# Optimization experiments

Measured on AMD Instinct MI355X. Metric: run time of the kernel, lower is better.

Reference implementation:

```python
import jax, jax.numpy as jnp
import numpy as np

N_NODES = 50000
N_EDGES = 400000
DIMS = 32
HEADS = 6
FEAT = DIMS * HEADS  # 192
NEG_SLOPE = 0.2  # PyG GATv2Conv default


def glorot(key, shape):
    fan_in, fan_out = shape[0], shape[1]
    lim = jnp.sqrt(6.0 / (fan_in + fan_out))
    return jax.random.uniform(key, shape, jnp.float32, -lim, lim)


def setup_inputs() -> dict:
    key = jax.random.key(0)
    ks = jax.random.split(key, 10)
    x = jax.random.normal(ks[0], (N_NODES, FEAT), jnp.float32)
    edge_index = jax.random.randint(ks[1], (2, N_EDGES), 0, N_NODES, jnp.int32)
    edge_weights = jax.random.uniform(ks[2], (N_EDGES, 1), jnp.float32)
    W_l = glorot(ks[3], (FEAT, FEAT))   # lin_l: in -> heads*out
    b_l = jnp.zeros((FEAT,), jnp.float32)
    W_r = glorot(ks[4], (FEAT, FEAT))   # lin_r (share_weights=False)
    b_r = jnp.zeros((FEAT,), jnp.float32)
    W_edge = glorot(ks[5], (1, FEAT))   # lin_edge: edge_dim=1 -> heads*out, no bias
    att = glorot(ks[6], (HEADS, DIMS))  # attention vector per head
    bias = jnp.zeros((FEAT,), jnp.float32)
    return {"x": x, "edge_index": edge_index, "edge_weights": edge_weights,
            "W_l": W_l, "b_l": b_l, "W_r": W_r, "b_r": b_r,
            "W_edge": W_edge, "att": att, "bias": bias}


def gatv2_res(x, edge_index, edge_weights, W_l, b_l, W_r, b_r, W_edge, att, bias):
    N = x.shape[0]
    H, C = att.shape
    src0, dst0 = edge_index[0], edge_index[1]

    # add_self_loops with fill_value='mean': self-loop attr = mean of edge_attr over incoming edges
    cnt = jax.ops.segment_sum(jnp.ones((edge_weights.shape[0],), x.dtype), dst0, num_segments=N)
    loop_attr = jax.ops.segment_sum(edge_weights, dst0, num_segments=N) / jnp.maximum(cnt, 1.0)[:, None]
    loops = jnp.arange(N, dtype=src0.dtype)
    src = jnp.concatenate([src0, loops])
    dst = jnp.concatenate([dst0, loops])
    e_attr = jnp.concatenate([edge_weights, loop_attr], axis=0)  # [E+N, 1]

    x_l = (x @ W_l + b_l).reshape(N, H, C)  # source transform
    x_r = (x @ W_r + b_r).reshape(N, H, C)  # target transform
    e_emb = (e_attr @ W_edge).reshape(-1, H, C)

    # per-edge GATv2 score
    m = jax.nn.leaky_relu(x_l[src] + x_r[dst] + e_emb, NEG_SLOPE)  # [E+N, H, C]
    alpha = jnp.einsum('ehc,hc->eh', m, att)  # [E+N, H]

    # segment softmax over edges incident to each target node (self-loops guarantee coverage)
    amax = jax.lax.stop_gradient(jax.ops.segment_max(alpha, dst, num_segments=N))
    ex = jnp.exp(alpha - amax[dst])
    denom = jax.ops.segment_sum(ex, dst, num_segments=N)
    a = ex / denom[dst]  # [E+N, H]

    out = jax.ops.segment_sum(x_l[src] * a[..., None], dst, num_segments=N)  # [N, H, C]
    out = out.reshape(N, H * C) + bias

    # ResLayer: residual + ReLU (dropout = identity in eval mode)
    return jax.nn.relu(x + out)


def reference(x, edge_index, edge_weights, W_l, b_l, W_r, b_r, W_edge, att, bias):
    return gatv2_res(x, edge_index, edge_weights, W_l, b_l, W_r, b_r, W_edge, att, bias)
```

## Files before the change

kernel.cpp:

```cpp
#include <hip/hip_runtime.h>
#include <hip/hip_bf16.h>
#include <math.h>

#define N_NODES 50000
#define N_EDGES 400000
#define HEADS 6
#define DIMS 32
#define FEAT 192
#define NEG_SLOPE 0.2f

typedef __attribute__((ext_vector_type(8))) short short8;
typedef __attribute__((ext_vector_type(4))) float f32x4;

__device__ __forceinline__ unsigned short f2bu(float f) {
    __hip_bfloat16 h = __float2bfloat16(f);
    unsigned short u; __builtin_memcpy(&u, &h, 2); return u;
}
__device__ __forceinline__ float bu2f(unsigned short u) {
    return __uint_as_float(((unsigned)u) << 16);
}

#define XL_OFF    0
#define XR_OFF    19200000
#define WT_OFF    38400000
#define BLR_OFF   38547456
#define PAIR_OFF  38548992
#define DEG_OFF   41748992
#define SCAN_OFF  42148992
#define BSUM_OFF  42348992
#define BOFF_OFF  42350016
#define NB_SCAN ((N_NODES + 255) / 256)

__global__ __launch_bounds__(256) void k_count(const int* __restrict__ ei,
                                               int* __restrict__ deg,
                                               const float* __restrict__ Wl,
                                               const float* __restrict__ Wr,
                                               const float* __restrict__ bl,
                                               const float* __restrict__ br,
                                               short* __restrict__ Wt,
                                               float* __restrict__ blr) {
    int e = blockIdx.x * blockDim.x + threadIdx.x;
    if (e < N_EDGES) atomicAdd(&deg[ei[N_EDGES + e]], 1);
    if (e < 384 * FEAT) {
        int n = e / FEAT, k = e - n * FEAT;
        float v = (n < FEAT) ? Wl[k * FEAT + n] : Wr[k * FEAT + (n - FEAT)];
        Wt[n * FEAT + k] = (short)f2bu(v);
    }
    if (e < 384) blr[e] = (e < FEAT) ? bl[e] : br[e - FEAT];
}

__global__ __launch_bounds__(256) void k_scan1(const int* __restrict__ deg,
                                               int* __restrict__ scan,
                                               int* __restrict__ bsums) {
    int t = threadIdx.x;
    int i = blockIdx.x * 256 + t;
    int v = (i < N_NODES) ? deg[i] : 0;
    __shared__ int s[256];
    s[t] = v; __syncthreads();
    for (int off = 1; off < 256; off <<= 1) {
        int u = (t >= off) ? s[t - off] : 0;
        __syncthreads();
        s[t] += u;
        __syncthreads();
    }
    if (i < N_NODES) scan[i] = s[t];
    if (t == 255) bsums[blockIdx.x] = s[255];
}

__global__ __launch_bounds__(256) void k_scan2(int* __restrict__ bsums,
                                               int* __restrict__ boffs) {
    int t = threadIdx.x;
    int v = (t < NB_SCAN) ? bsums[t] : 0;
    __shared__ int s[256];
    s[t] = v; __syncthreads();
    for (int off = 1; off < 256; off <<= 1) {
        int u = (t >= off) ? s[t - off] : 0;
        __syncthreads();
        s[t] += u;
        __syncthreads();
    }
    boffs[t] = s[t] - v;
}

#define SCAT_BLOCKS ((N_EDGES + 383) / 384)
#define GEMM_BLOCKS (N_NODES / 16)
#define OSTRIDE 392
#define ASTRIDE 200
__global__ __launch_bounds__(384) void k_scatgemm(const int* __restrict__ ei,
                                                  const float* __restrict__ ew,
                                                  const int* __restrict__ scan,
                                                  const int* __restrict__ boffs,
                                                  int* __restrict__ deg,
                                                  int2* __restrict__ pair,
                                                  const float* __restrict__ x,
                                                  const short* __restrict__ Wt,
                                                  const float* __restrict__ blr,
                                                  unsigned short* __restrict__ xl,
                                                  unsigned short* __restrict__ xr) {
    __shared__ unsigned short sOut[16 * OSTRIDE];
    __shared__ unsigned short sA[16 * ASTRIDE];
    if (blockIdx.x < SCAT_BLOCKS) {
        int e = blockIdx.x * 384 + threadIdx.x;
        if (e < N_EDGES) {
            int d = ei[N_EDGES + e];
            int inclEnd = boffs[d >> 8] + scan[d];
            int old = atomicSub(&deg[d], 1);
            int2 p; p.x = ei[e]; p.y = __float_as_int(ew[e]);
            pair[inclEnd - old] = p;
        }
        return;
    }
    size_t row0 = (size_t)(blockIdx.x - SCAT_BLOCKS) * 16;

    {
        int q = threadIdx.x;
        int row = q / 24, k0 = (q - row * 24) * 8;
        const float* ap = x + (row0 + row) * FEAT + k0;
        float4 v0 = *(const float4*)ap;
        float4 v1 = *(const float4*)(ap + 4);
        unsigned short tmp[8];
        tmp[0] = f2bu(v0.x); tmp[1] = f2bu(v0.y); tmp[2] = f2bu(v0.z); tmp[3] = f2bu(v0.w);
        tmp[4] = f2bu(v1.x); tmp[5] = f2bu(v1.y); tmp[6] = f2bu(v1.z); tmp[7] = f2bu(v1.w);
        int kw = (k0 >> 1) ^ ((row & 7) << 2);
        *(uint4*)&sA[row * ASTRIDE + kw * 2] = *(const uint4*)tmp;
    }
    __syncthreads();

    int wv   = threadIdx.x >> 6;
    int lane = threadIdx.x & 63;
    int m    = lane & 15;
    int kg   = lane >> 4;
    int ncol0 = wv * 64;

    f32x4 acc0 = {0.f,0.f,0.f,0.f}, acc1 = acc0, acc2 = acc0, acc3 = acc0;

#pragma unroll
    for (int ks = 0; ks < 6; ks++) {
        int kb = ks * 32 + kg * 8;
        int kw = (kb >> 1) ^ ((m & 7) << 2);
        short8 af = *(const short8*)&sA[m * ASTRIDE + kw * 2];
        const short* wp = Wt + (size_t)(ncol0 + m) * FEAT + kb;
        short8 b0 = *(const short8*)(wp);
        short8 b1 = *(const short8*)(wp + 16 * FEAT);
        short8 b2 = *(const short8*)(wp + 32 * FEAT);
        short8 b3 = *(const short8*)(wp + 48 * FEAT);
        acc0 = __builtin_amdgcn_mfma_f32_16x16x32_bf16(af, b0, acc0, 0, 0, 0);
        acc1 = __builtin_amdgcn_mfma_f32_16x16x32_bf16(af, b1, acc1, 0, 0, 0);
        acc2 = __builtin_amdgcn_mfma_f32_16x16x32_bf16(af, b2, acc2, 0, 0, 0);
        acc3 = __builtin_amdgcn_mfma_f32_16x16x32_bf16(af, b3, acc3, 0, 0, 0);
    }

    f32x4 accs[4] = {acc0, acc1, acc2, acc3};
#pragma unroll
    for (int t4 = 0; t4 < 4; t4++) {
        int cc = ncol0 + t4 * 16 + m;
        float bv = blr[cc];
#pragma unroll
        for (int r = 0; r < 4; r++) {
            sOut[(kg * 4 + r) * OSTRIDE + cc] = f2bu(accs[t4][r] + bv);
        }
    }
    __syncthreads();
    for (int q = threadIdx.x; q < 768; q += 384) {
        int row = q / 48, p = q - row * 48;
        uint4 v = *(const uint4*)&sOut[row * OSTRIDE + p * 8];
        if (p < 24) *(uint4*)(xl + (row0 + row) * FEAT + p * 8) = v;
        else        *(uint4*)(xr + (row0 + row) * FEAT + (p - 24) * 8) = v;
    }
}

#define NPB 8
#define CEDGE 32
#define RS 100
#define APAD 36
__global__ __launch_bounds__(192) void k_node(const float* __restrict__ x,
                                              const float* __restrict__ bias,
                                              const float* __restrict__ att,
                                              const float* __restrict__ We,
                                              const int* __restrict__ scan,
                                              const int* __restrict__ boffs,
                                              const int2* __restrict__ pair,
                                              const unsigned short* __restrict__ xl,
                                              const unsigned short* __restrict__ xr,
                                              float* __restrict__ out) {
    __shared__ __align__(16) unsigned int sXL[CEDGE * RS];
    __shared__ __align__(16) unsigned int sXR[NPB * RS];
    __shared__ float sEx[CEDGE * HEADS];
    __shared__ float sExS[NPB * HEADS];
    __shared__ int   sSrc[2][CEDGE];
    __shared__ float sW[2][CEDGE];
    __shared__ int   sDst[2][CEDGE];
    __shared__ int   sStart[NPB + 1];
    __shared__ __align__(16) float sAttP[HEADS * APAD];
    __shared__ __align__(16) float sWeP[HEADS * APAD];
    __shared__ float sDen[NPB * HEADS];
    __shared__ float sWsm[NPB];

    int t = threadIdx.x;
    int h = t >> 5;
    int n0 = blockIdx.x * NPB;

    int gbase = boffs[n0 >> 8] + ((n0 & 255) ? scan[n0 - 1] : 0);
    int n8 = n0 + NPB;
    int gend = (n8 >= N_NODES) ? N_EDGES
             : (boffs[n8 >> 8] + ((n8 & 255) ? scan[n8 - 1] : 0));
    int etot = gend - gbase;
    int c0 = min(etot, CEDGE);

    if (t < c0) { int2 p = pair[gbase + t]; sSrc[0][t] = p.x; sW[0][t] = __int_as_float(p.y); }

    for (int q = t; q < HEADS * APAD; q += 192) {
        int hh = q / APAD, c = q - hh * APAD;
        if (c < 32) { sAttP[q] = att[hh * 32 + c]; sWeP[q] = We[hh * 32 + c]; }
    }
    if (t <= NPB) {
        int n = n0 + t;
        int st;
        if (n >= N_NODES) st = N_EDGES;
        else {
            int b = n >> 8;
            st = boffs[b] + ((n & 255) ? scan[n - 1] : 0);
        }
        sStart[t] = st;
    }
    if (t < NPB) {
        int n = n0 + t;
        int a = boffs[n >> 8] + ((n & 255) ? scan[n - 1] : 0);
        int n1 = n + 1;
        int b = (n1 >= N_NODES) ? N_EDGES
              : (boffs[n1 >> 8] + ((n1 & 255) ? scan[n1 - 1] : 0));
        int lo = a - gbase; if (lo < 0) lo = 0;
        int hi = b - gbase; if (hi > c0) hi = c0;
        for (int q = lo; q < hi; q++) sDst[0][q] = t;
    }
    {
        int nn = t / 24, p = t - nn * 24;
        *(uint4*)&sXR[nn * RS + p * 4] = ((const uint4*)(xr + (size_t)(n0 + nn) * FEAT))[p];
    }
    __syncthreads();

    float acc[NPB];
#pragma unroll
    for (int nn = 0; nn < NPB; nn++) acc[nn] = 0.f;
    float redR = 0.f;
    int nnD = t / HEADS, hhD = t - nnD * HEADS;

    int nch = (etot + CEDGE - 1) / CEDGE;
    for (int ci = 0; ci < nch; ci++) {
        int i0 = ci * CEDGE;
        int c  = min(etot - i0, CEDGE);
        int cn = min(etot - i0 - CEDGE, CEDGE);
        int cb = ci & 1, nb = cb ^ 1;

        {
            int nld = c * 24;
#pragma unroll
            for (int s = 0; s < 4; s++) {
                int q = t + s * 192;
                if (q < nld) {
                    int i = q / 24, p = q - i * 24;
                    *(uint4*)&sXL[i * RS + p * 4] =
                        *(const uint4*)(xl + (size_t)sSrc[cb][i] * FEAT + p * 8);
                }
            }
        }
        int2 P;
        if (t < cn) P = pair[gbase + i0 + CEDGE + t];
        if (t < NPB && cn > 0) {
            int lo = sStart[t] - gbase - i0 - CEDGE;     if (lo < 0) lo = 0;
            int hi = sStart[t + 1] - gbase - i0 - CEDGE; if (hi > cn) hi = cn;
            for (int q = lo; q < hi; q++) sDst[nb][q] = t;
        }
        __syncthreads();

        if (t < c * HEADS) {
            int i = t / HEADS, hh = t - i * HEADS;
            int nn = sDst[cb][i];
            float w = sW[cb][i];
            const uint4* pa = (const uint4*)&sXL[i * RS + hh * 16];
            const uint4* pb = (const uint4*)&sXR[nn * RS + hh * 16];
            float alpha0 = 0.f, alpha1 = 0.f;
#pragma unroll
            for (int g = 0; g < 4; g++) {
                uint4 a4 = pa[g];
                uint4 b4 = pb[g];
                float4 we0 = *(const float4*)&sWeP[hh * APAD + g * 8];
                float4 we1 = *(const float4*)&sWeP[hh * APAD + g * 8 + 4];
                float4 at0 = *(const float4*)&sAttP[hh * APAD + g * 8];
                float4 at1 = *(const float4*)&sAttP[hh * APAD + g * 8 + 4];
                float wec[8] = {we0.x, we0.y, we0.z, we0.w, we1.x, we1.y, we1.z, we1.w};
                float atc[8] = {at0.x, at0.y, at0.z, at0.w, at1.x, at1.y, at1.z, at1.w};
                unsigned aw[4] = {a4.x, a4.y, a4.z, a4.w};
                unsigned bw[4] = {b4.x, b4.y, b4.z, b4.w};
#pragma unroll
                for (int q = 0; q < 4; q++) {
                    float m0 = bu2f((unsigned short)aw[q]) + bu2f((unsigned short)bw[q]) + w * wec[q * 2];
                    m0 = fmaxf(m0, NEG_SLOPE * m0);
                    alpha0 += m0 * atc[q * 2];
                    float m1 = bu2f((unsigned short)(aw[q] >> 16)) + bu2f((unsigned short)(bw[q] >> 16)) + w * wec[q * 2 + 1];
                    m1 = fmaxf(m1, NEG_SLOPE * m1);
                    alpha1 += m1 * atc[q * 2 + 1];
                }
            }
            sEx[t] = __expf(alpha0 + alpha1);
        }
        if (t < cn) { sSrc[nb][t] = P.x; sW[nb][t] = __int_as_float(P.y); }
        __syncthreads();

        {
            int cw = t >> 1;
#pragma unroll
            for (int nn = 0; nn < NPB; nn++) {
                int lo = sStart[nn] - gbase - i0;     if (lo < 0) lo = 0;
                int hi = sStart[nn + 1] - gbase - i0; if (hi > c) hi = c;
                int i = lo;
                for (; i + 1 < hi; i += 2) {
                    float ex0 = sEx[i * HEADS + h];
                    float ex1 = sEx[(i + 1) * HEADS + h];
                    unsigned u0 = sXL[i * RS + cw];
                    unsigned u1 = sXL[(i + 1) * RS + cw];
                    unsigned short v0 = (t & 1) ? (unsigned short)(u0 >> 16) : (unsigned short)u0;
                    unsigned short v1 = (t & 1) ? (unsigned short)(u1 >> 16) : (unsigned short)u1;
                    acc[nn] += ex0 * bu2f(v0) + ex1 * bu2f(v1);
                }
                if (i < hi) {
                    float ex = sEx[i * HEADS + h];
                    unsigned u = sXL[i * RS + cw];
                    unsigned short v = (t & 1) ? (unsigned short)(u >> 16) : (unsigned short)u;
                    acc[nn] += ex * bu2f(v);
                }
            }
            if (t < NPB * HEADS) {
                int lo = sStart[nnD] - gbase - i0;     if (lo < 0) lo = 0;
                int hi = sStart[nnD + 1] - gbase - i0; if (hi > c) hi = c;
                int i = lo;
                for (; i + 1 < hi; i += 2)
                    redR += sEx[i * HEADS + hhD] + sEx[(i + 1) * HEADS + hhD];
                if (i < hi) redR += sEx[i * HEADS + hhD];
            } else if (t < NPB * HEADS + NPB) {
                int nw = t - NPB * HEADS;
                int lo = sStart[nw] - gbase - i0;     if (lo < 0) lo = 0;
                int hi = sStart[nw + 1] - gbase - i0; if (hi > c) hi = c;
                for (int i = lo; i < hi; i++) redR += sW[cb][i];
            }
        }
        __syncthreads();
    }

    if (t < NPB * HEADS) sDen[t] = redR;
    else if (t < NPB * HEADS + NPB) sWsm[t - NPB * HEADS] = redR;
    __syncthreads();

    if (t < NPB * HEADS) {
        int nn = nnD, hh = hhD;
        int dg = sStart[nn + 1] - sStart[nn];
        float w = sWsm[nn] / fmaxf((float)dg, 1.0f);
        const uint4* pa = (const uint4*)(xl + (size_t)(n0 + nn) * FEAT + hh * 32);
        const uint4* pb = (const uint4*)&sXR[nn * RS + hh * 16];
        float alpha0 = 0.f, alpha1 = 0.f;
#pragma unroll
        for (int g = 0; g < 4; g++) {
            uint4 a4 = pa[g];
            uint4 b4 = pb[g];
            float4 we0 = *(const float4*)&sWeP[hh * APAD + g * 8];
            float4 we1 = *(const float4*)&sWeP[hh * APAD + g * 8 + 4];
            float4 at0 = *(const float4*)&sAttP[hh * APAD + g * 8];
            float4 at1 = *(const float4*)&sAttP[hh * APAD + g * 8 + 4];
            float wec[8] = {we0.x, we0.y, we0.z, we0.w, we1.x, we1.y, we1.z, we1.w};
            float atc[8] = {at0.x, at0.y, at0.z, at0.w, at1.x, at1.y, at1.z, at1.w};
            unsigned aw[4] = {a4.x, a4.y, a4.z, a4.w};
            unsigned bw[4] = {b4.x, b4.y, b4.z, b4.w};
#pragma unroll
            for (int q = 0; q < 4; q++) {
                float m0 = bu2f((unsigned short)aw[q]) + bu2f((unsigned short)bw[q]) + w * wec[q * 2];
                m0 = fmaxf(m0, NEG_SLOPE * m0);
                alpha0 += m0 * atc[q * 2];
                float m1 = bu2f((unsigned short)(aw[q] >> 16)) + bu2f((unsigned short)(bw[q] >> 16)) + w * wec[q * 2 + 1];
                m1 = fmaxf(m1, NEG_SLOPE * m1);
                alpha1 += m1 * atc[q * 2 + 1];
            }
        }
        sExS[t] = __expf(alpha0 + alpha1);
    }
    __syncthreads();

    {
        float bj = bias[t];
#pragma unroll
        for (int nn = 0; nn < NPB; nn++) {
            float exS = sExS[nn * HEADS + h];
            size_t off = (size_t)(n0 + nn) * FEAT + t;
            float xsv = bu2f(xl[off]);
            float num = acc[nn] + exS * xsv;
            float dn  = sDen[nn * HEADS + h] + exS;
            float val = x[off] + bj + num / dn;
            out[off] = (val > 0.f) ? val : 0.f;
        }
    }
}

extern "C" void kernel_launch(void* const* d_in, const int* in_sizes, int n_in,
                              void* d_out, int out_size, void* d_ws, size_t ws_size,
                              hipStream_t stream) {
    const float* x    = (const float*)d_in[0];
    const int*   ei   = (const int*)d_in[1];
    const float* ew   = (const float*)d_in[2];
    const float* Wl   = (const float*)d_in[3];
    const float* bl   = (const float*)d_in[4];
    const float* Wr   = (const float*)d_in[5];
    const float* br   = (const float*)d_in[6];
    const float* We   = (const float*)d_in[7];
    const float* att  = (const float*)d_in[8];
    const float* bias = (const float*)d_in[9];
    float* out = (float*)d_out;

    char* ws = (char*)d_ws;
    unsigned short* xl = (unsigned short*)(ws + XL_OFF);
    unsigned short* xr = (unsigned short*)(ws + XR_OFF);
    short* Wt     = (short*)(ws + WT_OFF);
    float* blr    = (float*)(ws + BLR_OFF);
    int2*  pair   = (int2*)(ws + PAIR_OFF);
    int*   deg    = (int*)(ws + DEG_OFF);
    int*   scan   = (int*)(ws + SCAN_OFF);
    int*   bsums  = (int*)(ws + BSUM_OFF);
    int*   boffs  = (int*)(ws + BOFF_OFF);

    hipMemsetAsync(ws + DEG_OFF, 0, N_NODES * sizeof(int), stream);

    k_count<<<(N_EDGES + 255) / 256, 256, 0, stream>>>(ei, deg, Wl, Wr, bl, br, Wt, blr);
    k_scan1<<<NB_SCAN, 256, 0, stream>>>(deg, scan, bsums);
    k_scan2<<<1, 256, 0, stream>>>(bsums, boffs);

    k_scatgemm<<<SCAT_BLOCKS + GEMM_BLOCKS, 384, 0, stream>>>(ei, ew, scan, boffs, deg,
                                                              pair, x, Wt, blr, xl, xr);

    k_node<<<N_NODES / NPB, 192, 0, stream>>>(x, bias, att, We, scan, boffs,
                                              pair, xl, xr, out);
}
```

Before: 284.7 us.

## Precompute scatter cursors, double GEMM rows per block, de-unroll aggregation loops

Adds a k_fix kernel that writes each node's inclusive end offset into deg, so the scatter atomically decrements a cursor and no longer reads the scan and block-offset arrays per edge. The GEMM part now handles 32 rows per block instead of 16, reusing each loaded weight fragment across two A tiles with guarded edge rows. The 2-way manual unroll in the node aggregation and denominator loops is replaced by simple loops. This costs one extra kernel launch and more registers per GEMM thread.

```diff
diff --git a/kernel.cpp b/kernel.cpp
--- a/kernel.cpp
+++ b/kernel.cpp
@@ -82,14 +82,19 @@
     boffs[t] = s[t] - v;
 }
 
+__global__ __launch_bounds__(256) void k_fix(int* __restrict__ deg,
+                                             const int* __restrict__ scan,
+                                             const int* __restrict__ boffs) {
+    int i = blockIdx.x * 256 + threadIdx.x;
+    if (i < N_NODES) deg[i] = boffs[i >> 8] + scan[i];
+}
+
 #define SCAT_BLOCKS ((N_EDGES + 383) / 384)
-#define GEMM_BLOCKS (N_NODES / 16)
+#define GEMM_BLOCKS ((N_NODES + 31) / 32)
 #define OSTRIDE 392
 #define ASTRIDE 200
 __global__ __launch_bounds__(384) void k_scatgemm(const int* __restrict__ ei,
                                                   const float* __restrict__ ew,
-                                                  const int* __restrict__ scan,
-                                                  const int* __restrict__ boffs,
                                                   int* __restrict__ deg,
                                                   int2* __restrict__ pair,
                                                   const float* __restrict__ x,
@@ -98,24 +103,25 @@
                                                   unsigned short* __restrict__ xl,
                                                   unsigned short* __restrict__ xr) {
     __shared__ unsigned short sOut[16 * OSTRIDE];
-    __shared__ unsigned short sA[16 * ASTRIDE];
+    __shared__ unsigned short sA[32 * ASTRIDE];
     if (blockIdx.x < SCAT_BLOCKS) {
         int e = blockIdx.x * 384 + threadIdx.x;
         if (e < N_EDGES) {
             int d = ei[N_EDGES + e];
-            int inclEnd = boffs[d >> 8] + scan[d];
             int old = atomicSub(&deg[d], 1);
             int2 p; p.x = ei[e]; p.y = __float_as_int(ew[e]);
-            pair[inclEnd - old] = p;
+            pair[old - 1] = p;
         }
         return;
     }
-    size_t row0 = (size_t)(blockIdx.x - SCAT_BLOCKS) * 16;
-
-    {
-        int q = threadIdx.x;
+    size_t row0 = (size_t)(blockIdx.x - SCAT_BLOCKS) * 32;
+
+#pragma unroll
+    for (int s = 0; s < 2; s++) {
+        int q = threadIdx.x + s * 384;
         int row = q / 24, k0 = (q - row * 24) * 8;
-        const float* ap = x + (row0 + row) * FEAT + k0;
+        size_t gr = row0 + row;
+        const float* ap = x + (gr < N_NODES ? gr : row0) * FEAT + k0;
         float4 v0 = *(const float4*)ap;
         float4 v1 = *(const float4*)(ap + 4);
         unsigned short tmp[8];
@@ -132,40 +138,55 @@
     int kg   = lane >> 4;
     int ncol0 = wv * 64;
 
-    f32x4 acc0 = {0.f,0.f,0.f,0.f}, acc1 = acc0, acc2 = acc0, acc3 = acc0;
+    f32x4 acc[2][4];
+#pragma unroll
+    for (int r = 0; r < 2; r++)
+#pragma unroll
+        for (int j = 0; j < 4; j++) acc[r][j] = (f32x4){0.f, 0.f, 0.f, 0.f};
 
 #pragma unroll
     for (int ks = 0; ks < 6; ks++) {
         int kb = ks * 32 + kg * 8;
         int kw = (kb >> 1) ^ ((m & 7) << 2);
-        short8 af = *(const short8*)&sA[m * ASTRIDE + kw * 2];
+        short8 af0 = *(const short8*)&sA[m * ASTRIDE + kw * 2];
+        short8 af1 = *(const short8*)&sA[(16 + m) * ASTRIDE + kw * 2];
         const short* wp = Wt + (size_t)(ncol0 + m) * FEAT + kb;
         short8 b0 = *(const short8*)(wp);
         short8 b1 = *(const short8*)(wp + 16 * FEAT);
         short8 b2 = *(const short8*)(wp + 32 * FEAT);
         short8 b3 = *(const short8*)(wp + 48 * FEAT);
-        acc0 = __builtin_amdgcn_mfma_f32_16x16x32_bf16(af, b0, acc0, 0, 0, 0);
-        acc1 = __builtin_amdgcn_mfma_f32_16x16x32_bf16(af, b1, acc1, 0, 0, 0);
-        acc2 = __builtin_amdgcn_mfma_f32_16x16x32_bf16(af, b2, acc2, 0, 0, 0);
-        acc3 = __builtin_amdgcn_mfma_f32_16x16x32_bf16(af, b3, acc3, 0, 0, 0);
-    }
-
-    f32x4 accs[4] = {acc0, acc1, acc2, acc3};
-#pragma unroll
-    for (int t4 = 0; t4 < 4; t4++) {
-        int cc = ncol0 + t4 * 16 + m;
-        float bv = blr[cc];
-#pragma unroll
-        for (int r = 0; r < 4; r++) {
-            sOut[(kg * 4 + r) * OSTRIDE + cc] = f2bu(accs[t4][r] + bv);
-        }
-    }
-    __syncthreads();
-    for (int q = threadIdx.x; q < 768; q += 384) {
-        int row = q / 48, p = q - row * 48;
-        uint4 v = *(const uint4*)&sOut[row * OSTRIDE + p * 8];
-        if (p < 24) *(uint4*)(xl + (row0 + row) * FEAT + p * 8) = v;
-        else        *(uint4*)(xr + (row0 + row) * FEAT + (p - 24) * 8) = v;
+        acc[0][0] = __builtin_amdgcn_mfma_f32_16x16x32_bf16(af0, b0, acc[0][0], 0, 0, 0);
+        acc[0][1] = __builtin_amdgcn_mfma_f32_16x16x32_bf16(af0, b1, acc[0][1], 0, 0, 0);
+        acc[0][2] = __builtin_amdgcn_mfma_f32_16x16x32_bf16(af0, b2, acc[0][2], 0, 0, 0);
+        acc[0][3] = __builtin_amdgcn_mfma_f32_16x16x32_bf16(af0, b3, acc[0][3], 0, 0, 0);
+        acc[1][0] = __builtin_amdgcn_mfma_f32_16x16x32_bf16(af1, b0, acc[1][0], 0, 0, 0);
+        acc[1][1] = __builtin_amdgcn_mfma_f32_16x16x32_bf16(af1, b1, acc[1][1], 0, 0, 0);
+        acc[1][2] = __builtin_amdgcn_mfma_f32_16x16x32_bf16(af1, b2, acc[1][2], 0, 0, 0);
+        acc[1][3] = __builtin_amdgcn_mfma_f32_16x16x32_bf16(af1, b3, acc[1][3], 0, 0, 0);
+    }
+
+#pragma unroll
+    for (int pass = 0; pass < 2; pass++) {
+        if (pass) __syncthreads();
+#pragma unroll
+        for (int t4 = 0; t4 < 4; t4++) {
+            int cc = ncol0 + t4 * 16 + m;
+            float bv = blr[cc];
+#pragma unroll
+            for (int r = 0; r < 4; r++) {
+                sOut[(kg * 4 + r) * OSTRIDE + cc] = f2bu(acc[pass][t4][r] + bv);
+            }
+        }
+        __syncthreads();
+        for (int q = threadIdx.x; q < 768; q += 384) {
+            int row = q / 48, p = q - row * 48;
+            size_t gr = row0 + pass * 16 + row;
+            if (gr < N_NODES) {
+                uint4 v = *(const uint4*)&sOut[row * OSTRIDE + p * 8];
+                if (p < 24) *(uint4*)(xl + gr * FEAT + p * 8) = v;
+                else        *(uint4*)(xr + gr * FEAT + (p - 24) * 8) = v;
+            }
+        }
     }
 }
 
@@ -313,17 +334,7 @@
             for (int nn = 0; nn < NPB; nn++) {
                 int lo = sStart[nn] - gbase - i0;     if (lo < 0) lo = 0;
                 int hi = sStart[nn + 1] - gbase - i0; if (hi > c) hi = c;
-                int i = lo;
-                for (; i + 1 < hi; i += 2) {
-                    float ex0 = sEx[i * HEADS + h];
-                    float ex1 = sEx[(i + 1) * HEADS + h];
-                    unsigned u0 = sXL[i * RS + cw];
-                    unsigned u1 = sXL[(i + 1) * RS + cw];
-                    unsigned short v0 = (t & 1) ? (unsigned short)(u0 >> 16) : (unsigned short)u0;
-                    unsigned short v1 = (t & 1) ? (unsigned short)(u1 >> 16) : (unsigned short)u1;
-                    acc[nn] += ex0 * bu2f(v0) + ex1 * bu2f(v1);
-                }
-                if (i < hi) {
+                for (int i = lo; i < hi; i++) {
                     float ex = sEx[i * HEADS + h];
                     unsigned u = sXL[i * RS + cw];
                     unsigned short v = (t & 1) ? (unsigned short)(u >> 16) : (unsigned short)u;
@@ -333,10 +344,7 @@
             if (t < NPB * HEADS) {
                 int lo = sStart[nnD] - gbase - i0;     if (lo < 0) lo = 0;
                 int hi = sStart[nnD + 1] - gbase - i0; if (hi > c) hi = c;
-                int i = lo;
-                for (; i + 1 < hi; i += 2)
-                    redR += sEx[i * HEADS + hhD] + sEx[(i + 1) * HEADS + hhD];
-                if (i < hi) redR += sEx[i * HEADS + hhD];
+                for (int i = lo; i < hi; i++) redR += sEx[i * HEADS + hhD];
             } else if (t < NPB * HEADS + NPB) {
                 int nw = t - NPB * HEADS;
                 int lo = sStart[nw] - gbase - i0;     if (lo < 0) lo = 0;
@@ -430,9 +438,10 @@
     k_count<<<(N_EDGES + 255) / 256, 256, 0, stream>>>(ei, deg, Wl, Wr, bl, br, Wt, blr);
     k_scan1<<<NB_SCAN, 256, 0, stream>>>(deg, scan, bsums);
     k_scan2<<<1, 256, 0, stream>>>(bsums, boffs);
-
-    k_scatgemm<<<SCAT_BLOCKS + GEMM_BLOCKS, 384, 0, stream>>>(ei, ew, scan, boffs, deg,
-                                                              pair, x, Wt, blr, xl, xr);
+    k_fix<<<NB_SCAN, 256, 0, stream>>>(deg, scan, boffs);
+
+    k_scatgemm<<<SCAT_BLOCKS + GEMM_BLOCKS, 384, 0, stream>>>(ei, ew, deg, pair,
+                                                              x, Wt, blr, xl, xr);
 
     k_node<<<N_NODES / NPB, 192, 0, stream>>>(x, bias, att, We, scan, boffs,
                                               pair, xl, xr, out);
```

Measured after the change: 273.9 us. -3.8%, faster.
